# Kernel optimization log

Hardware: AMD Instinct MI355X
Metric: run time of the kernel (lower is better)

Reference implementation:

```python
import jax, jax.numpy as jnp
import numpy as np

N_EMBD = 64
N_HEADS = 8
HEAD_SIZE = N_EMBD // N_HEADS  # 8
HIDDEN = 32 * N_EMBD           # 2048
BLOCK = 256
EPS = 1e-5


def setup_inputs() -> dict:
    key = jax.random.key(0)
    ks = jax.random.split(key, 12)
    B, T = 512, 256
    s_in = 1.0 / np.sqrt(N_EMBD)
    s_hid = 1.0 / np.sqrt(HIDDEN)
    return {
        "x": jax.random.normal(ks[0], (B, T, N_EMBD), jnp.float32),
        # per-head Q/K/V projections stacked over heads: [H, D, E]
        "Wq": jax.random.normal(ks[1], (N_HEADS, N_EMBD, HEAD_SIZE), jnp.float32) * s_in,
        "bq": jnp.zeros((N_HEADS, HEAD_SIZE), jnp.float32),
        "Wk": jax.random.normal(ks[2], (N_HEADS, N_EMBD, HEAD_SIZE), jnp.float32) * s_in,
        "bk": jnp.zeros((N_HEADS, HEAD_SIZE), jnp.float32),
        "Wv": jax.random.normal(ks[3], (N_HEADS, N_EMBD, HEAD_SIZE), jnp.float32) * s_in,
        "bv": jnp.zeros((N_HEADS, HEAD_SIZE), jnp.float32),
        "Wp": jax.random.normal(ks[4], (N_EMBD, N_EMBD), jnp.float32) * s_in,
        "bp": jnp.zeros((N_EMBD,), jnp.float32),
        "g1": jnp.ones((N_EMBD,), jnp.float32),
        "beta1": jnp.zeros((N_EMBD,), jnp.float32),
        "W1": jax.random.normal(ks[5], (N_EMBD, HIDDEN), jnp.float32) * s_in,
        "b1": jnp.zeros((HIDDEN,), jnp.float32),
        "W2": jax.random.normal(ks[6], (HIDDEN, N_EMBD), jnp.float32) * s_hid,
        "b2": jnp.zeros((N_EMBD,), jnp.float32),
        "g2": jnp.ones((N_EMBD,), jnp.float32),
        "beta2": jnp.zeros((N_EMBD,), jnp.float32),
    }


def _layernorm(x, g, b):
    mu = jnp.mean(x, axis=-1, keepdims=True)
    var = jnp.mean(jnp.square(x - mu), axis=-1, keepdims=True)
    return (x - mu) * jax.lax.rsqrt(var + EPS) * g + b


def reference(x, Wq, bq, Wk, bk, Wv, bv, Wp, bp, g1, beta1, W1, b1, W2, b2, g2, beta2):
    B, T, D = x.shape
    # batched multi-head causal attention (equivalent to per-head loop)
    q = jnp.einsum('btd,hde->bhte', x, Wq) + bq[None, :, None, :]
    k = jnp.einsum('btd,hde->bhte', x, Wk) + bk[None, :, None, :]
    v = jnp.einsum('btd,hde->bhte', x, Wv) + bv[None, :, None, :]
    scores = jnp.einsum('bhte,bhse->bhts', q, k) / np.sqrt(HEAD_SIZE)
    causal = jnp.tril(jnp.ones((T, T), bool))
    scores = jnp.where(causal, scores, -jnp.inf)
    attn = jax.nn.softmax(scores, axis=-1)
    o = jnp.einsum('bhts,bhse->bhte', attn, v)          # [B,H,T,E]
    o = o.transpose(0, 2, 1, 3).reshape(B, T, D)        # concat heads
    attn_out = o @ Wp + bp
    h = _layernorm(x + attn_out, g1, beta1)
    ff = jax.nn.relu(h @ W1 + b1) @ W2 + b2
    return _layernorm(h + ff, g2, beta2)
```

## Files before the change

kernel.cpp:

```cpp
#include <hip/hip_runtime.h>

#define B_    512
#define T_    256
#define D_    64
#define H_    8
#define E_    8
#define HID_  2048
#define EPS_  1e-5f
#define SCALE_ 0.3535533905932738f

__global__ __launch_bounds__(256) void attn_k(
    const float* __restrict__ x,
    const float* __restrict__ Wq, const float* __restrict__ bq,
    const float* __restrict__ Wk, const float* __restrict__ bk,
    const float* __restrict__ Wv, const float* __restrict__ bv,
    float* __restrict__ o_ws)
{
  __shared__ __align__(16) float xs[64][68];
  __shared__ __align__(16) float qs[256][8], ks[256][8], vs[256][8];
  __shared__ __align__(16) float wqs[512], wks[512], wvs[512];
  __shared__ float bqs[8], bks[8], bvs[8];

  const int tid = threadIdx.x;
  const int b = blockIdx.x >> 3, h = blockIdx.x & 7;

  for (int i = tid; i < 512; i += 256) {
    wqs[i] = Wq[h * 512 + i];
    wks[i] = Wk[h * 512 + i];
    wvs[i] = Wv[h * 512 + i];
  }
  if (tid < 8) {
    bqs[tid] = bq[h * 8 + tid];
    bks[tid] = bk[h * 8 + tid];
    bvs[tid] = bv[h * 8 + tid];
  }

  const int e = tid & 7, tg = tid >> 3;
  for (int ch = 0; ch < 4; ++ch) {
    {
      const int r = tid >> 2, cq = tid & 3;
      const float* xrow = x + ((size_t)b * T_ + ch * 64 + r) * D_ + cq * 16;
      float* dst = &xs[r][cq * 16];
      #pragma unroll
      for (int c = 0; c < 4; ++c)
        *(float4*)&dst[c * 4] = *(const float4*)&xrow[c * 4];
    }
    __syncthreads();
    #pragma unroll
    for (int i = 0; i < 2; ++i) {
      const int tl = tg + 32 * i, t = ch * 64 + tl;
      float aq = bqs[e], ak = bks[e], av = bvs[e];
      #pragma unroll
      for (int c = 0; c < 16; ++c) {
        float4 xv = *(const float4*)&xs[tl][c * 4];
        const int d = c * 4;
        aq += xv.x * wqs[(d + 0) * 8 + e] + xv.y * wqs[(d + 1) * 8 + e]
            + xv.z * wqs[(d + 2) * 8 + e] + xv.w * wqs[(d + 3) * 8 + e];
        ak += xv.x * wks[(d + 0) * 8 + e] + xv.y * wks[(d + 1) * 8 + e]
            + xv.z * wks[(d + 2) * 8 + e] + xv.w * wks[(d + 3) * 8 + e];
        av += xv.x * wvs[(d + 0) * 8 + e] + xv.y * wvs[(d + 1) * 8 + e]
            + xv.z * wvs[(d + 2) * 8 + e] + xv.w * wvs[(d + 3) * 8 + e];
      }
      qs[t][e] = aq * SCALE_;
      ks[t][e] = ak;
      vs[t][e] = av;
    }
    __syncthreads();
  }

  {
    const int t = tid;
    float4 q0 = *(const float4*)&qs[t][0];
    float4 q1 = *(const float4*)&qs[t][4];
    float m = -INFINITY, l = 0.f;
    float o0 = 0, o1 = 0, o2 = 0, o3 = 0, o4 = 0, o5 = 0, o6 = 0, o7 = 0;
    for (int s = 0; s <= t; ++s) {
      float4 ka = *(const float4*)&ks[s][0];
      float4 kb = *(const float4*)&ks[s][4];
      float sc = q0.x * ka.x + q0.y * ka.y + q0.z * ka.z + q0.w * ka.w
               + q1.x * kb.x + q1.y * kb.y + q1.z * kb.z + q1.w * kb.w;
      float mn = fmaxf(m, sc);
      float corr = __expf(m - mn);
      float p = __expf(sc - mn);
      m = mn;
      l = l * corr + p;
      float4 va = *(const float4*)&vs[s][0];
      float4 vb = *(const float4*)&vs[s][4];
      o0 = o0 * corr + p * va.x;  o1 = o1 * corr + p * va.y;
      o2 = o2 * corr + p * va.z;  o3 = o3 * corr + p * va.w;
      o4 = o4 * corr + p * vb.x;  o5 = o5 * corr + p * vb.y;
      o6 = o6 * corr + p * vb.z;  o7 = o7 * corr + p * vb.w;
    }
    float inv = 1.f / l;
    float* orow = o_ws + ((size_t)b * T_ + t) * D_ + h * E_;
    float4 r0 = { o0 * inv, o1 * inv, o2 * inv, o3 * inv };
    float4 r1 = { o4 * inv, o5 * inv, o6 * inv, o7 * inv };
    *(float4*)&orow[0] = r0;
    *(float4*)&orow[4] = r1;
  }
}

__global__ __launch_bounds__(256) void proj_ln1_k(
    const float* __restrict__ x,
    const float* __restrict__ Wp, const float* __restrict__ bp,
    const float* __restrict__ g1, const float* __restrict__ be1,
    const float* __restrict__ o_ws, float* __restrict__ h_ws)
{
  __shared__ __align__(16) float os[32][68];
  __shared__ __align__(16) float wps[4096];
  const int tid = threadIdx.x;
  const size_t t0 = (size_t)blockIdx.x * 32;

  {
    const int t = tid >> 3, c = tid & 7;
    const float* orow = o_ws + (t0 + t) * D_ + c * 8;
    *(float4*)&os[t][c * 8 + 0] = *(const float4*)&orow[0];
    *(float4*)&os[t][c * 8 + 4] = *(const float4*)&orow[4];
  }
  #pragma unroll
  for (int c = 0; c < 4; ++c)
    ((float4*)wps)[tid + 256 * c] = ((const float4*)Wp)[tid + 256 * c];
  __syncthreads();

  const int t = tid >> 3, tl = tid & 7, d0 = tl * 8;
  float acc[8];
  {
    float4 b0 = *(const float4*)&bp[d0];
    float4 b1v = *(const float4*)&bp[d0 + 4];
    acc[0] = b0.x; acc[1] = b0.y; acc[2] = b0.z; acc[3] = b0.w;
    acc[4] = b1v.x; acc[5] = b1v.y; acc[6] = b1v.z; acc[7] = b1v.w;
  }
  for (int i = 0; i < 64; ++i) {
    float ov = os[t][i];
    const float* wr = &wps[i * 64 + d0];
    float4 w0 = *(const float4*)wr;
    float4 w1 = *(const float4*)(wr + 4);
    acc[0] += ov * w0.x; acc[1] += ov * w0.y; acc[2] += ov * w0.z; acc[3] += ov * w0.w;
    acc[4] += ov * w1.x; acc[5] += ov * w1.y; acc[6] += ov * w1.z; acc[7] += ov * w1.w;
  }
  float r[8];
  {
    const float* xrow = x + (t0 + t) * D_ + d0;
    float4 x0 = *(const float4*)&xrow[0];
    float4 x1 = *(const float4*)&xrow[4];
    r[0] = x0.x + acc[0]; r[1] = x0.y + acc[1]; r[2] = x0.z + acc[2]; r[3] = x0.w + acc[3];
    r[4] = x1.x + acc[4]; r[5] = x1.y + acc[5]; r[6] = x1.z + acc[6]; r[7] = x1.w + acc[7];
  }
  float s1 = 0.f, s2 = 0.f;
  #pragma unroll
  for (int k = 0; k < 8; ++k) { s1 += r[k]; s2 += r[k] * r[k]; }
  #pragma unroll
  for (int mM = 1; mM < 8; mM <<= 1) {
    s1 += __shfl_xor(s1, mM, 8);
    s2 += __shfl_xor(s2, mM, 8);
  }
  float mu = s1 * (1.f / 64.f);
  float var = s2 * (1.f / 64.f) - mu * mu;
  float rstd = rsqrtf(var + EPS_);
  float4 g0 = *(const float4*)&g1[d0];
  float4 g1v = *(const float4*)&g1[d0 + 4];
  float4 e0 = *(const float4*)&be1[d0];
  float4 e1 = *(const float4*)&be1[d0 + 4];
  float4 h0, h1;
  h0.x = (r[0] - mu) * rstd * g0.x + e0.x;
  h0.y = (r[1] - mu) * rstd * g0.y + e0.y;
  h0.z = (r[2] - mu) * rstd * g0.z + e0.z;
  h0.w = (r[3] - mu) * rstd * g0.w + e0.w;
  h1.x = (r[4] - mu) * rstd * g1v.x + e1.x;
  h1.y = (r[5] - mu) * rstd * g1v.y + e1.y;
  h1.z = (r[6] - mu) * rstd * g1v.z + e1.z;
  h1.w = (r[7] - mu) * rstd * g1v.w + e1.w;
  float* hrow = h_ws + (t0 + t) * D_ + d0;
  *(float4*)&hrow[0] = h0;
  *(float4*)&hrow[4] = h1;
}

__global__ __launch_bounds__(256, 3) void ffn_ln2_k(
    const float* __restrict__ W1, const float* __restrict__ b1,
    const float* __restrict__ W2, const float* __restrict__ b2,
    const float* __restrict__ g2, const float* __restrict__ be2,
    const float* __restrict__ h_ws, float* __restrict__ out)
{
  __shared__ __align__(16) float ht[64][32];
  __shared__ __align__(16) float hid[32][260];
  const int tid = threadIdx.x;
  const size_t t0 = (size_t)blockIdx.x * 32;

  {
    const int t = tid >> 3, ds = (tid & 7) * 8;
    const float* hrow = h_ws + (t0 + t) * D_ + ds;
    float4 a = *(const float4*)hrow;
    float4 b = *(const float4*)(hrow + 4);
    ht[ds + 0][t] = a.x; ht[ds + 1][t] = a.y; ht[ds + 2][t] = a.z; ht[ds + 3][t] = a.w;
    ht[ds + 4][t] = b.x; ht[ds + 5][t] = b.y; ht[ds + 6][t] = b.z; ht[ds + 7][t] = b.w;
  }

  const int mg  = tid >> 6;
  const int ng  = tid & 63;
  const int kq  = tid >> 6;
  const int mg2 = (tid >> 3) & 7;
  const int ng2 = tid & 7;

  float acc2[4][8];
  #pragma unroll
  for (int i = 0; i < 4; ++i)
    #pragma unroll
    for (int d = 0; d < 8; ++d) acc2[i][d] = 0.f;

  __syncthreads();

  for (int ch = 0; ch < 8; ++ch) {
    const int c0 = ch * 256;

    float acc1[8][4];
    {
      float4 bb = *(const float4*)&b1[c0 + ng * 4];
      #pragma unroll
      for (int i = 0; i < 8; ++i) {
        acc1[i][0] = bb.x; acc1[i][1] = bb.y; acc1[i][2] = bb.z; acc1[i][3] = bb.w;
      }
    }
    const float* w1p = W1 + c0 + ng * 4;
    #pragma unroll 4
    for (int k = 0; k < 64; ++k) {
      float4 w  = *(const float4*)&w1p[(size_t)k * HID_];
      float4 a0 = *(const float4*)&ht[k][mg * 8];
      float4 a1 = *(const float4*)&ht[k][mg * 8 + 4];
      float am[8], wv[4];
      *(float4*)&am[0] = a0; *(float4*)&am[4] = a1;
      *(float4*)&wv[0] = w;
      #pragma unroll
      for (int i = 0; i < 8; ++i)
        #pragma unroll
        for (int c = 0; c < 4; ++c)
          acc1[i][c] += am[i] * wv[c];
    }
    #pragma unroll
    for (int i = 0; i < 8; ++i) {
      float4 r;
      r.x = fmaxf(acc1[i][0], 0.f); r.y = fmaxf(acc1[i][1], 0.f);
      r.z = fmaxf(acc1[i][2], 0.f); r.w = fmaxf(acc1[i][3], 0.f);
      *(float4*)&hid[mg * 8 + i][ng * 4] = r;
    }
    __syncthreads();

    const float* w2p = W2 + ((size_t)c0 + (size_t)kq * 64) * D_ + ng2 * 8;
    #pragma unroll 2
    for (int kk = 0; kk < 64; kk += 4) {
      const int j = kq * 64 + kk;
      float hv[4][4];
      #pragma unroll
      for (int i = 0; i < 4; ++i)
        *(float4*)&hv[i][0] = *(const float4*)&hid[mg2 * 4 + i][j];
      const float* wp = w2p + (size_t)kk * D_;
      #pragma unroll
      for (int u = 0; u < 4; ++u) {
        float4 w0  = *(const float4*)&wp[u * D_];
        float4 w1v = *(const float4*)&wp[u * D_ + 4];
        #pragma unroll
        for (int i = 0; i < 4; ++i) {
          const float h = hv[i][u];
          acc2[i][0] += h * w0.x;  acc2[i][1] += h * w0.y;
          acc2[i][2] += h * w0.z;  acc2[i][3] += h * w0.w;
          acc2[i][4] += h * w1v.x; acc2[i][5] += h * w1v.y;
          acc2[i][6] += h * w1v.z; acc2[i][7] += h * w1v.w;
        }
      }
    }
    __syncthreads();
  }

  {
    float* red = &hid[0][0];
    #pragma unroll
    for (int i = 0; i < 4; ++i) {
      float* dst = red + (size_t)(kq * 32 + mg2 * 4 + i) * 64 + ng2 * 8;
      float4 r0 = { acc2[i][0], acc2[i][1], acc2[i][2], acc2[i][3] };
      float4 r1 = { acc2[i][4], acc2[i][5], acc2[i][6], acc2[i][7] };
      *(float4*)&dst[0] = r0;
      *(float4*)&dst[4] = r1;
    }
  }
  __syncthreads();

  {
    const float* red = &hid[0][0];
    const int tf = tid >> 3, df = (tid & 7) * 8;
    float r[8];
    {
      float4 s0 = *(const float4*)&red[(size_t)tf * 64 + df];
      float4 s1v = *(const float4*)&red[(size_t)tf * 64 + df + 4];
      #pragma unroll
      for (int q = 1; q < 4; ++q) {
        float4 a0 = *(const float4*)&red[((size_t)q * 32 + tf) * 64 + df];
        float4 a1 = *(const float4*)&red[((size_t)q * 32 + tf) * 64 + df + 4];
        s0.x += a0.x; s0.y += a0.y; s0.z += a0.z; s0.w += a0.w;
        s1v.x += a1.x; s1v.y += a1.y; s1v.z += a1.z; s1v.w += a1.w;
      }
      float4 b0 = *(const float4*)&b2[df];
      float4 b1v = *(const float4*)&b2[df + 4];
      r[0] = s0.x + b0.x + ht[df + 0][tf];
      r[1] = s0.y + b0.y + ht[df + 1][tf];
      r[2] = s0.z + b0.z + ht[df + 2][tf];
      r[3] = s0.w + b0.w + ht[df + 3][tf];
      r[4] = s1v.x + b1v.x + ht[df + 4][tf];
      r[5] = s1v.y + b1v.y + ht[df + 5][tf];
      r[6] = s1v.z + b1v.z + ht[df + 6][tf];
      r[7] = s1v.w + b1v.w + ht[df + 7][tf];
    }
    float s1 = 0.f, s2 = 0.f;
    #pragma unroll
    for (int k = 0; k < 8; ++k) { s1 += r[k]; s2 += r[k] * r[k]; }
    #pragma unroll
    for (int mM = 1; mM < 8; mM <<= 1) {
      s1 += __shfl_xor(s1, mM, 8);
      s2 += __shfl_xor(s2, mM, 8);
    }
    float mu = s1 * (1.f / 64.f);
    float var = s2 * (1.f / 64.f) - mu * mu;
    float rstd = rsqrtf(var + EPS_);
    float4 g0 = *(const float4*)&g2[df];
    float4 g1v = *(const float4*)&g2[df + 4];
    float4 e0 = *(const float4*)&be2[df];
    float4 e1 = *(const float4*)&be2[df + 4];
    float4 o0, o1;
    o0.x = (r[0] - mu) * rstd * g0.x + e0.x;
    o0.y = (r[1] - mu) * rstd * g0.y + e0.y;
    o0.z = (r[2] - mu) * rstd * g0.z + e0.z;
    o0.w = (r[3] - mu) * rstd * g0.w + e0.w;
    o1.x = (r[4] - mu) * rstd * g1v.x + e1.x;
    o1.y = (r[5] - mu) * rstd * g1v.y + e1.y;
    o1.z = (r[6] - mu) * rstd * g1v.z + e1.z;
    o1.w = (r[7] - mu) * rstd * g1v.w + e1.w;
    float* orow = out + (t0 + tf) * D_ + df;
    *(float4*)&orow[0] = o0;
    *(float4*)&orow[4] = o1;
  }
}

extern "C" void kernel_launch(void* const* d_in, const int* in_sizes, int n_in,
                              void* d_out, int out_size, void* d_ws, size_t ws_size,
                              hipStream_t stream) {
  const float* x   = (const float*)d_in[0];
  const float* Wq  = (const float*)d_in[1];
  const float* bq  = (const float*)d_in[2];
  const float* Wk  = (const float*)d_in[3];
  const float* bk  = (const float*)d_in[4];
  const float* Wv  = (const float*)d_in[5];
  const float* bv  = (const float*)d_in[6];
  const float* Wp  = (const float*)d_in[7];
  const float* bp  = (const float*)d_in[8];
  const float* g1  = (const float*)d_in[9];
  const float* be1 = (const float*)d_in[10];
  const float* W1  = (const float*)d_in[11];
  const float* b1  = (const float*)d_in[12];
  const float* W2  = (const float*)d_in[13];
  const float* b2  = (const float*)d_in[14];
  const float* g2  = (const float*)d_in[15];
  const float* be2 = (const float*)d_in[16];
  float* out = (float*)d_out;

  float* o_ws = (float*)d_ws;
  float* h_ws = o_ws + (size_t)B_ * T_ * D_;

  attn_k<<<B_ * H_, 256, 0, stream>>>(x, Wq, bq, Wk, bk, Wv, bv, o_ws);
  proj_ln1_k<<<(B_ * T_) / 32, 256, 0, stream>>>(x, Wp, bp, g1, be1, o_ws, h_ws);
  ffn_ln2_k<<<(B_ * T_) / 32, 256, 0, stream>>>(W1, b1, W2, b2, g2, be2, h_ws, out);
}
```

Before: 1.276 ms.

## Make FFN wave-local to drop block barriers and reduce via shuffles

Restructures the FFN kernel so each wavefront owns its own 8 tokens through both the W1 and W2 stages. Each wave then reads only the hidden rows it wrote itself, which removes the per-chunk __syncthreads. The cross-k-split partial sums are now reduced with wavefront shuffles instead of an LDS reduction buffer plus barrier, and the residual is re-read from global memory. The 3-blocks occupancy hint is dropped from launch bounds. The trade-off is more shuffle work and duplicated LayerNorm math across the k-split lanes, with a possible register-pressure change.

```diff
diff --git a/kernel.cpp b/kernel.cpp
--- a/kernel.cpp
+++ b/kernel.cpp
@@ -175,15 +175,17 @@
   *(float4*)&hrow[4] = h1;
 }
 
-__global__ __launch_bounds__(256, 3) void ffn_ln2_k(
+__global__ __launch_bounds__(256) void ffn_ln2_k(
     const float* __restrict__ W1, const float* __restrict__ b1,
     const float* __restrict__ W2, const float* __restrict__ b2,
-    const float* __restrict__ g2, const float* __restrict__ be2,
+    const float* __restrict__ g2p, const float* __restrict__ be2,
     const float* __restrict__ h_ws, float* __restrict__ out)
 {
   __shared__ __align__(16) float ht[64][32];
   __shared__ __align__(16) float hid[32][260];
+
   const int tid = threadIdx.x;
+  const int wv = tid >> 6, lane = tid & 63;
   const size_t t0 = (size_t)blockIdx.x * 32;
 
   {
@@ -194,20 +196,18 @@
     ht[ds + 0][t] = a.x; ht[ds + 1][t] = a.y; ht[ds + 2][t] = a.z; ht[ds + 3][t] = a.w;
     ht[ds + 4][t] = b.x; ht[ds + 5][t] = b.y; ht[ds + 6][t] = b.z; ht[ds + 7][t] = b.w;
   }
-
-  const int mg  = tid >> 6;
-  const int ng  = tid & 63;
-  const int kq  = tid >> 6;
-  const int mg2 = (tid >> 3) & 7;
-  const int ng2 = tid & 7;
-
-  float acc2[4][8];
+  __syncthreads();
+
+  const int ng = lane;
+  const int kq = lane >> 4;
+  const int tp = (lane >> 3) & 1;
+  const int dg = lane & 7;
+
+  float accO[4][8];
   #pragma unroll
   for (int i = 0; i < 4; ++i)
     #pragma unroll
-    for (int d = 0; d < 8; ++d) acc2[i][d] = 0.f;
-
-  __syncthreads();
+    for (int d = 0; d < 8; ++d) accO[i][d] = 0.f;
 
   for (int ch = 0; ch < 8; ++ch) {
     const int c0 = ch * 256;
@@ -224,35 +224,33 @@
     #pragma unroll 4
     for (int k = 0; k < 64; ++k) {
       float4 w  = *(const float4*)&w1p[(size_t)k * HID_];
-      float4 a0 = *(const float4*)&ht[k][mg * 8];
-      float4 a1 = *(const float4*)&ht[k][mg * 8 + 4];
-      float am[8], wv[4];
+      float4 a0 = *(const float4*)&ht[k][wv * 8];
+      float4 a1 = *(const float4*)&ht[k][wv * 8 + 4];
+      float am[8], wvv[4];
       *(float4*)&am[0] = a0; *(float4*)&am[4] = a1;
-      *(float4*)&wv[0] = w;
+      *(float4*)&wvv[0] = w;
       #pragma unroll
       for (int i = 0; i < 8; ++i)
         #pragma unroll
         for (int c = 0; c < 4; ++c)
-          acc1[i][c] += am[i] * wv[c];
+          acc1[i][c] += am[i] * wvv[c];
     }
     #pragma unroll
     for (int i = 0; i < 8; ++i) {
       float4 r;
       r.x = fmaxf(acc1[i][0], 0.f); r.y = fmaxf(acc1[i][1], 0.f);
       r.z = fmaxf(acc1[i][2], 0.f); r.w = fmaxf(acc1[i][3], 0.f);
-      *(float4*)&hid[mg * 8 + i][ng * 4] = r;
-    }
-    __syncthreads();
-
-    const float* w2p = W2 + ((size_t)c0 + (size_t)kq * 64) * D_ + ng2 * 8;
+      *(float4*)&hid[wv * 8 + i][ng * 4] = r;
+    }
+
     #pragma unroll 2
     for (int kk = 0; kk < 64; kk += 4) {
-      const int j = kq * 64 + kk;
+      const int jc = kq * 64 + kk;
       float hv[4][4];
       #pragma unroll
       for (int i = 0; i < 4; ++i)
-        *(float4*)&hv[i][0] = *(const float4*)&hid[mg2 * 4 + i][j];
-      const float* wp = w2p + (size_t)kk * D_;
+        *(float4*)&hv[i][0] = *(const float4*)&hid[wv * 8 + tp * 4 + i][jc];
+      const float* wp = W2 + (size_t)(c0 + jc) * D_ + dg * 8;
       #pragma unroll
       for (int u = 0; u < 4; ++u) {
         float4 w0  = *(const float4*)&wp[u * D_];
@@ -260,81 +258,68 @@
         #pragma unroll
         for (int i = 0; i < 4; ++i) {
           const float h = hv[i][u];
-          acc2[i][0] += h * w0.x;  acc2[i][1] += h * w0.y;
-          acc2[i][2] += h * w0.z;  acc2[i][3] += h * w0.w;
-          acc2[i][4] += h * w1v.x; acc2[i][5] += h * w1v.y;
-          acc2[i][6] += h * w1v.z; acc2[i][7] += h * w1v.w;
+          accO[i][0] += h * w0.x;  accO[i][1] += h * w0.y;
+          accO[i][2] += h * w0.z;  accO[i][3] += h * w0.w;
+          accO[i][4] += h * w1v.x; accO[i][5] += h * w1v.y;
+          accO[i][6] += h * w1v.z; accO[i][7] += h * w1v.w;
         }
       }
     }
-    __syncthreads();
-  }
-
-  {
-    float* red = &hid[0][0];
+  }
+
+  #pragma unroll
+  for (int mM = 16; mM <= 32; mM <<= 1)
+    #pragma unroll
+    for (int i = 0; i < 4; ++i)
+      #pragma unroll
+      for (int d = 0; d < 8; ++d)
+        accO[i][d] += __shfl_xor(accO[i][d], mM, 64);
+
+  {
+    const int d0 = dg * 8;
+    float4 b2a = *(const float4*)&b2[d0];
+    float4 b2b = *(const float4*)&b2[d0 + 4];
+    float4 g0 = *(const float4*)&g2p[d0];
+    float4 g1v = *(const float4*)&g2p[d0 + 4];
+    float4 e0 = *(const float4*)&be2[d0];
+    float4 e1 = *(const float4*)&be2[d0 + 4];
     #pragma unroll
     for (int i = 0; i < 4; ++i) {
-      float* dst = red + (size_t)(kq * 32 + mg2 * 4 + i) * 64 + ng2 * 8;
-      float4 r0 = { acc2[i][0], acc2[i][1], acc2[i][2], acc2[i][3] };
-      float4 r1 = { acc2[i][4], acc2[i][5], acc2[i][6], acc2[i][7] };
-      *(float4*)&dst[0] = r0;
-      *(float4*)&dst[4] = r1;
-    }
-  }
-  __syncthreads();
-
-  {
-    const float* red = &hid[0][0];
-    const int tf = tid >> 3, df = (tid & 7) * 8;
-    float r[8];
-    {
-      float4 s0 = *(const float4*)&red[(size_t)tf * 64 + df];
-      float4 s1v = *(const float4*)&red[(size_t)tf * 64 + df + 4];
-      #pragma unroll
-      for (int q = 1; q < 4; ++q) {
-        float4 a0 = *(const float4*)&red[((size_t)q * 32 + tf) * 64 + df];
-        float4 a1 = *(const float4*)&red[((size_t)q * 32 + tf) * 64 + df + 4];
-        s0.x += a0.x; s0.y += a0.y; s0.z += a0.z; s0.w += a0.w;
-        s1v.x += a1.x; s1v.y += a1.y; s1v.z += a1.z; s1v.w += a1.w;
-      }
-      float4 b0 = *(const float4*)&b2[df];
-      float4 b1v = *(const float4*)&b2[df + 4];
-      r[0] = s0.x + b0.x + ht[df + 0][tf];
-      r[1] = s0.y + b0.y + ht[df + 1][tf];
-      r[2] = s0.z + b0.z + ht[df + 2][tf];
-      r[3] = s0.w + b0.w + ht[df + 3][tf];
-      r[4] = s1v.x + b1v.x + ht[df + 4][tf];
-      r[5] = s1v.y + b1v.y + ht[df + 5][tf];
-      r[6] = s1v.z + b1v.z + ht[df + 6][tf];
-      r[7] = s1v.w + b1v.w + ht[df + 7][tf];
-    }
-    float s1 = 0.f, s2 = 0.f;
-    #pragma unroll
-    for (int k = 0; k < 8; ++k) { s1 += r[k]; s2 += r[k] * r[k]; }
-    #pragma unroll
-    for (int mM = 1; mM < 8; mM <<= 1) {
-      s1 += __shfl_xor(s1, mM, 8);
-      s2 += __shfl_xor(s2, mM, 8);
-    }
-    float mu = s1 * (1.f / 64.f);
-    float var = s2 * (1.f / 64.f) - mu * mu;
-    float rstd = rsqrtf(var + EPS_);
-    float4 g0 = *(const float4*)&g2[df];
-    float4 g1v = *(const float4*)&g2[df + 4];
-    float4 e0 = *(const float4*)&be2[df];
-    float4 e1 = *(const float4*)&be2[df + 4];
-    float4 o0, o1;
-    o0.x = (r[0] - mu) * rstd * g0.x + e0.x;
-    o0.y = (r[1] - mu) * rstd * g0.y + e0.y;
-    o0.z = (r[2] - mu) * rstd * g0.z + e0.z;
-    o0.w = (r[3] - mu) * rstd * g0.w + e0.w;
-    o1.x = (r[4] - mu) * rstd * g1v.x + e1.x;
-    o1.y = (r[5] - mu) * rstd * g1v.y + e1.y;
-    o1.z = (r[6] - mu) * rstd * g1v.z + e1.z;
-    o1.w = (r[7] - mu) * rstd * g1v.w + e1.w;
-    float* orow = out + (t0 + tf) * D_ + df;
-    *(float4*)&orow[0] = o0;
-    *(float4*)&orow[4] = o1;
+      const int tok = wv * 8 + tp * 4 + i;
+      const float* hrow = h_ws + (t0 + tok) * D_ + d0;
+      float4 h0 = *(const float4*)&hrow[0];
+      float4 h1 = *(const float4*)&hrow[4];
+      float r[8];
+      r[0] = accO[i][0] + b2a.x + h0.x;  r[1] = accO[i][1] + b2a.y + h0.y;
+      r[2] = accO[i][2] + b2a.z + h0.z;  r[3] = accO[i][3] + b2a.w + h0.w;
+      r[4] = accO[i][4] + b2b.x + h1.x;  r[5] = accO[i][5] + b2b.y + h1.y;
+      r[6] = accO[i][6] + b2b.z + h1.z;  r[7] = accO[i][7] + b2b.w + h1.w;
+      float s1 = 0.f, s2 = 0.f;
+      #pragma unroll
+      for (int k = 0; k < 8; ++k) { s1 += r[k]; s2 += r[k] * r[k]; }
+      #pragma unroll
+      for (int mM = 1; mM < 8; mM <<= 1) {
+        s1 += __shfl_xor(s1, mM, 8);
+        s2 += __shfl_xor(s2, mM, 8);
+      }
+      float mu = s1 * (1.f / 64.f);
+      float var = s2 * (1.f / 64.f) - mu * mu;
+      float rstd = rsqrtf(var + EPS_);
+      if (kq == 0) {
+        float4 o0, o1;
+        o0.x = (r[0] - mu) * rstd * g0.x + e0.x;
+        o0.y = (r[1] - mu) * rstd * g0.y + e0.y;
+        o0.z = (r[2] - mu) * rstd * g0.z + e0.z;
+        o0.w = (r[3] - mu) * rstd * g0.w + e0.w;
+        o1.x = (r[4] - mu) * rstd * g1v.x + e1.x;
+        o1.y = (r[5] - mu) * rstd * g1v.y + e1.y;
+        o1.z = (r[6] - mu) * rstd * g1v.z + e1.z;
+        o1.w = (r[7] - mu) * rstd * g1v.w + e1.w;
+        float* orow = out + (t0 + tok) * D_ + d0;
+        *(float4*)&orow[0] = o0;
+        *(float4*)&orow[4] = o1;
+      }
+    }
   }
 }
 
```

Result: slower. 1.372 ms (+7.6%).
